# Kernel tuning notes

Measured on AMD Instinct MI355X. Metric: run time of the kernel, lower is better.

The kernel has to match this reference:

```python
import jax, jax.numpy as jnp
import numpy as np

GROUPS = 32
EPS = 1e-5


def setup_inputs() -> dict:
    key = jax.random.key(0)
    ks = jax.random.split(key, 4)
    b, c, h, w = 4, 256, 64, 64
    x = jax.random.normal(ks[0], (b, c, h, w), dtype=jnp.float32)
    gn_gamma = jnp.ones((c,), dtype=jnp.float32)
    gn_beta = jnp.zeros((c,), dtype=jnp.float32)
    # 1x1 convs are pointwise linear maps: store kernels as [out, in]
    w_qkv = jax.random.normal(ks[1], (3 * c, c), dtype=jnp.float32) * (1.0 / np.sqrt(c))
    b_qkv = jnp.zeros((3 * c,), dtype=jnp.float32)
    w_out = jax.random.normal(ks[2], (c, c), dtype=jnp.float32) * (1.0 / np.sqrt(c))
    b_out = jnp.zeros((c,), dtype=jnp.float32)
    return {"x": x, "gn_gamma": gn_gamma, "gn_beta": gn_beta,
            "w_qkv": w_qkv, "b_qkv": b_qkv, "w_out": w_out, "b_out": b_out}


def reference(x, gn_gamma, gn_beta, w_qkv, b_qkv, w_out, b_out):
    b, c, h, w = x.shape
    # GroupNorm(32, c)
    xg = x.reshape(b, GROUPS, c // GROUPS, h, w)
    mean = jnp.mean(xg, axis=(2, 3, 4), keepdims=True)
    var = jnp.var(xg, axis=(2, 3, 4), keepdims=True)
    xn = ((xg - mean) * jax.lax.rsqrt(var + EPS)).reshape(b, c, h, w)
    xn = xn * gn_gamma[None, :, None, None] + gn_beta[None, :, None, None]
    # 1x1 conv QKV projection: [b, 3c, h, w]
    qkv = jnp.einsum('bchw,oc->bohw', xn, w_qkv) + b_qkv[None, :, None, None]
    q, k, v = jnp.split(qkv, 3, axis=1)
    n = h * w
    q = q.transpose(0, 2, 3, 1).reshape(b, n, c)  # [b, n, c]
    k = k.reshape(b, c, n)                        # [b, c, n]
    v = v.transpose(0, 2, 3, 1).reshape(b, n, c)  # [b, n, c]
    scores = jnp.einsum('bic,bcj->bij', q, k) * (c ** -0.5)  # [b, n, n]
    attn = jax.nn.softmax(scores, axis=-1)
    out = jnp.einsum('bij,bjc->bic', attn, v)     # [b, n, c]
    out = out.reshape(b, h, w, c).transpose(0, 3, 1, 2)  # [b, c, h, w]
    out = jnp.einsum('bchw,oc->bohw', out, w_out) + b_out[None, :, None, None]
    return out + x
```

## Files before the change

### kernel.cpp

```cpp
#include <hip/hip_runtime.h>
#include <hip/hip_bf16.h>
#include <cstdint>
#include <cstddef>

#define DEVINL __device__ __forceinline__

typedef unsigned short u16;
typedef unsigned char u8;
typedef unsigned int u32;
typedef __attribute__((ext_vector_type(8))) short short8;
typedef __attribute__((ext_vector_type(4))) float f32x4;
typedef __attribute__((ext_vector_type(4))) u16 u16x4;

constexpr int CH = 256;
constexpr int HW = 4096;
constexpr int NB = 4;
constexpr float M0L = 5.7707801636f;
constexpr float QKS = 0.3002805f;

DEVINL u16 f2bf(float f) {
  union { float f; u32 u; } v; v.f = f;
  u32 u = v.u;
  u32 r = u + 0x7FFFu + ((u >> 16) & 1u);
  return (u16)(r >> 16);
}
DEVINL float bf2f(u16 h) {
  union { u32 u; float f; } v; v.u = ((u32)h) << 16; return v.f;
}
DEVINL float fexp2(float x) {
  float r; asm("v_exp_f32 %0, %1" : "=v"(r) : "v"(x)); return r;
}
DEVINL u32 cvtpk(float lo, float hi) {
  u32 r; asm("v_cvt_pk_bf16_f32 %0, %1, %2" : "=v"(r) : "v"(lo), "v"(hi)); return r;
}
DEVINL u8 f2fp8(float v) {
  return (u8)(__builtin_amdgcn_cvt_pk_fp8_f32(v, v, 0, false) & 0xFF);
}
DEVINL void plswap(u32& a, u32& b) {
  asm("v_permlane32_swap_b32 %0, %1" : "+v"(a), "+v"(b));
  asm("v_permlane16_swap_b32 %0, %1" : "+v"(a), "+v"(b));
}

DEVINL void gl_lds16(const void* g, void* l) {
  __builtin_amdgcn_global_load_lds(
      (__attribute__((address_space(1))) void*)(size_t)g,
      (__attribute__((address_space(3))) void*)l, 16, 0, 0);
}

DEVINL f32x4 mfma_bf16(short8 a, short8 b, f32x4 c) {
  return __builtin_amdgcn_mfma_f32_16x16x32_bf16(a, b, c, 0, 0, 0);
}
DEVINL f32x4 mfma_fp8(long a, long b, f32x4 c) {
  return __builtin_amdgcn_mfma_f32_16x16x32_fp8_fp8(a, b, c, 0, 0, 0);
}

__global__ void k_pre(const float* __restrict__ x, float* __restrict__ stats,
                      const float* __restrict__ wq, const float* __restrict__ wo,
                      u16* __restrict__ w3, u16* __restrict__ wob) {
  if (blockIdx.x >= 128) {
    int i = (blockIdx.x - 128) * 256 + threadIdx.x;
    w3[i] = f2bf(wq[i]);
    if (i < 65536) wob[i] = f2bf(wo[i]);
    return;
  }
  int bg = blockIdx.x;
  const float* p = x + (size_t)bg * 32768;
  float s = 0.f, ss = 0.f;
  for (int i = threadIdx.x; i < 8192; i += 256) {
    float4 v = ((const float4*)p)[i];
    s += v.x + v.y + v.z + v.w;
    ss += v.x * v.x + v.y * v.y + v.z * v.z + v.w * v.w;
  }
  for (int m = 32; m; m >>= 1) { s += __shfl_xor(s, m); ss += __shfl_xor(ss, m); }
  __shared__ float rs[4], rss[4];
  int w = threadIdx.x >> 6;
  if ((threadIdx.x & 63) == 0) { rs[w] = s; rss[w] = ss; }
  __syncthreads();
  if (threadIdx.x == 0) {
    s = rs[0] + rs[1] + rs[2] + rs[3];
    ss = rss[0] + rss[1] + rss[2] + rss[3];
    float mean = s / 32768.f;
    float var = ss / 32768.f - mean * mean;
    stats[bg * 2] = mean;
    stats[bg * 2 + 1] = rsqrtf(var + 1e-5f);
  }
}

__global__ void k_norm(const float* __restrict__ x, const float* __restrict__ stats,
                       const float* __restrict__ gamma, const float* __restrict__ beta,
                       u16* __restrict__ xnT) {
  int bid = blockIdx.x;
  int b = bid >> 8, ct = (bid >> 6) & 3, pt = bid & 63;
  int c0 = ct * 64, p0 = pt * 64;
  __shared__ u16 tile[64][66];
  const float* xb = x + ((size_t)b * CH + c0) * HW + p0;
#pragma unroll
  for (int it = 0; it < 4; it++) {
    int li = threadIdx.x + it * 256;
    int ci = li >> 4, pq = (li & 15) * 4;
    float4 v = *(const float4*)(xb + (size_t)ci * HW + pq);
    int c = c0 + ci;
    int gg = c >> 3;
    float mean = stats[(b * 32 + gg) * 2], rstd = stats[(b * 32 + gg) * 2 + 1];
    float ga = gamma[c] * rstd;
    float be = beta[c] - mean * ga;
    tile[ci][pq + 0] = f2bf(v.x * ga + be);
    tile[ci][pq + 1] = f2bf(v.y * ga + be);
    tile[ci][pq + 2] = f2bf(v.z * ga + be);
    tile[ci][pq + 3] = f2bf(v.w * ga + be);
  }
  __syncthreads();
#pragma unroll
  for (int it = 0; it < 2; it++) {
    int ch = threadIdx.x + it * 256;
    int pr = ch >> 3, cc = (ch & 7) * 8;
    short8 res;
#pragma unroll
    for (int q2 = 0; q2 < 8; q2++) res[q2] = (short)tile[cc + q2][pr];
    *(short8*)(xnT + ((size_t)b * HW + p0 + pr) * CH + c0 + cc) = res;
  }
}

DEVINL void stage_tile(char* dst, const u16* src_rows, int kt, int w, int lane) {
#pragma unroll
  for (int it = 0; it < 4; it++) {
    int CI = w * 256 + it * 64 + lane;
    int row = CI >> 3, ci = CI & 7;
    int sci = ci ^ (row & 7);
    gl_lds16(src_rows + (size_t)row * 256 + kt * 64 + sci * 8,
             dst + w * 4096 + it * 1024);
  }
}

DEVINL short8 ldsA(const char* base, int row, int colb) {
  return *(const short8*)(base + row * 128 + (colb ^ ((row & 7) << 4)));
}

__global__ __launch_bounds__(256, 2) void k_qkv(
    const u16* __restrict__ xnT, const u16* __restrict__ w3,
    const float* __restrict__ bqkv,
    u8* __restrict__ Qg8, u8* __restrict__ Kg8, u16* __restrict__ Vg) {
  int bid = blockIdx.x;
  int b = bid / 192; int rm = bid - b * 192; int mt = rm / 6, nt = rm - mt * 6;
  extern __shared__ char sm[];
  const int tid = threadIdx.x, w = tid >> 6, lane = tid & 63, t = lane & 15, g = lane >> 4;
  const u16* Abase = xnT + ((size_t)b * HW + mt * 128) * CH;
  const u16* Bbase = w3 + (size_t)nt * 128 * CH;
  f32x4 acc[4][4] = {};
  stage_tile(sm, Abase, 0, w, lane);
  stage_tile(sm + 32768, Bbase, 0, w, lane);
  __syncthreads();
  for (int kt = 0; kt < 4; kt++) {
    int cur = kt & 1;
    if (kt < 3) {
      stage_tile(sm + ((cur ^ 1) * 16384), Abase, kt + 1, w, lane);
      stage_tile(sm + 32768 + ((cur ^ 1) * 16384), Bbase, kt + 1, w, lane);
    }
    const char* Asm = sm + cur * 16384;
    const char* Bsm = sm + 32768 + cur * 16384;
#pragma unroll
    for (int ks = 0; ks < 2; ks++) {
      short8 af[4], bf[4];
#pragma unroll
      for (int m = 0; m < 4; m++) af[m] = ldsA(Asm, 64 * (w >> 1) + 16 * m + t, ks * 64 + g * 16);
#pragma unroll
      for (int n = 0; n < 4; n++) bf[n] = ldsA(Bsm, 64 * (w & 1) + 16 * n + t, ks * 64 + g * 16);
#pragma unroll
      for (int m = 0; m < 4; m++)
#pragma unroll
        for (int n = 0; n < 4; n++)
          acc[m][n] = mfma_bf16(af[m], bf[n], acc[m][n]);
    }
    __syncthreads();
  }
#pragma unroll
  for (int n = 0; n < 4; n++) {
    int o = nt * 128 + 64 * (w & 1) + 16 * n + t;
    float bias = bqkv[o];
#pragma unroll
    for (int m = 0; m < 4; m++) {
      int p0 = mt * 128 + 64 * (w >> 1) + 16 * m + 4 * g;
      if (nt < 4) {
        u8* dst = (nt < 2) ? Qg8 : Kg8;
        int oo = (nt < 2) ? o : o - 256;
#pragma unroll
        for (int rr = 0; rr < 4; rr++) {
          float v = (acc[m][n][rr] + bias) * QKS;
          dst[((size_t)b * HW + p0 + rr) * CH + oo] = f2fp8(v);
        }
      } else {
        int oo = o - 512;
        u16x4 pv;
#pragma unroll
        for (int rr = 0; rr < 4; rr++) pv[rr] = f2bf(acc[m][n][rr] + bias);
        *(u16x4*)(Vg + (size_t)b * CH * HW + (size_t)oo * HW + p0) = pv;
      }
    }
  }
}

__global__ __launch_bounds__(512, 2) void k_attn(
    const u8* __restrict__ Qg8, const u8* __restrict__ Kg8, const u16* __restrict__ Vg,
    u16* __restrict__ Op, float* __restrict__ ml) {
  int bid = blockIdx.x;
  int qb = bid >> 4, b = (bid >> 2) & 3, split = bid & 3;
  extern __shared__ char sm[];
  const int tid = threadIdx.x, w = tid >> 6, lane = tid & 63, t = lane & 15, g = lane >> 4;
  const u8* Qb = Qg8 + (size_t)b * HW * CH;
  const u8* Kb = Kg8 + (size_t)b * HW * CH;
  const u16* Vb = Vg + (size_t)b * CH * HW;
  int qrow0 = qb * 256 + w * 32;
  int kv0 = split * 1024;

  long q8[2][8];
#pragma unroll
  for (int rf = 0; rf < 2; rf++)
#pragma unroll
    for (int ks = 0; ks < 8; ks++)
      q8[rf][ks] = *(const long*)(Qb + (size_t)(qrow0 + rf * 16 + t) * CH + ks * 32 + g * 8);

  f32x4 oacc[2][16] = {};
  float lsum[2] = {0.f, 0.f};
  f32x4 sf[2][4];
  short8 pf[2][2];

  int kOffB[2], vOffE[4];
#pragma unroll
  for (int it = 0; it < 2; it++) {
    int CI = w * 128 + it * 64 + lane;
    int row = CI >> 4, c = CI & 15;
    kOffB[it] = row * 256 + ((c ^ (row & 7)) * 16);
  }
#pragma unroll
  for (int it = 0; it < 4; it++) {
    int CI = w * 256 + it * 64 + lane;
    int rowv = CI >> 3, civ = CI & 7;
    vOffE[it] = rowv * HW + ((civ ^ (rowv & 7)) * 8);
  }
  auto stageKV = [&](int kbuf, int vbuf, int tt) {
    char* KL = sm + kbuf * 16384 + w * 2048;
    char* VL = sm + 32768 + vbuf * 32768 + w * 4096;
    const u8* ksrc = Kb + (size_t)(kv0 + tt * 64) * CH;
    const u16* vsrc = Vb + (kv0 + tt * 64);
#pragma unroll
    for (int it = 0; it < 2; it++) gl_lds16(ksrc + kOffB[it], KL + it * 1024);
#pragma unroll
    for (int it = 0; it < 4; it++) gl_lds16(vsrc + vOffE[it], VL + it * 1024);
  };

  auto QK = [&](const char* KL) {
#pragma unroll
    for (int jf = 0; jf < 4; jf++) {
      int row = jf * 16 + t;
      f32x4 a0 = {}, a1 = {};
#pragma unroll
      for (int ks = 0; ks < 8; ks++) {
        int s = ks * 4 + g;
        long kf = *(const long*)(KL + row * 256 + (((s >> 1) ^ (row & 7)) << 4) + ((s & 1) << 3));
        a0 = mfma_fp8(kf, q8[0][ks], a0);
        a1 = mfma_fp8(kf, q8[1][ks], a1);
      }
      sf[0][jf] = a0; sf[1][jf] = a1;
    }
  };
  auto PV = [&](const char* VL) {
#pragma unroll
    for (int ks = 0; ks < 2; ks++)
#pragma unroll
      for (int cf = 0; cf < 16; cf++) {
        int row = cf * 16 + t;
        short8 vf = *(const short8*)(VL + row * 128 + ((ks * 64 + g * 16) ^ ((row & 7) << 4)));
        oacc[0][cf] = mfma_bf16(pf[0][ks], vf, oacc[0][cf]);
        oacc[1][cf] = mfma_bf16(pf[1][ks], vf, oacc[1][cf]);
      }
  };
  auto SM = [&]() {
#pragma unroll
    for (int rf = 0; rf < 2; rf++) {
      u32 A[4][2];
#pragma unroll
      for (int jf = 0; jf < 4; jf++) {
        float e0 = fexp2(sf[rf][jf][0] - M0L);
        float e1 = fexp2(sf[rf][jf][1] - M0L);
        float e2 = fexp2(sf[rf][jf][2] - M0L);
        float e3 = fexp2(sf[rf][jf][3] - M0L);
        lsum[rf] += (e0 + e1) + (e2 + e3);
        A[jf][0] = cvtpk(e0, e1);
        A[jf][1] = cvtpk(e2, e3);
      }
#pragma unroll
      for (int ks = 0; ks < 2; ks++) {
        u32 X0 = A[2 * ks][0], Y0 = A[2 * ks + 1][0];
        u32 X1 = A[2 * ks][1], Y1 = A[2 * ks + 1][1];
        plswap(X0, Y0);
        plswap(X1, Y1);
        union { u32 u[4]; short8 s8; } pk;
        pk.u[0] = X0; pk.u[1] = X1; pk.u[2] = Y0; pk.u[3] = Y1;
        pf[rf][ks] = pk.s8;
      }
    }
  };

  stageKV(0, 0, 0);
  stageKV(1, 1, 1);
  asm volatile("s_waitcnt vmcnt(6)" ::: "memory");
  __builtin_amdgcn_s_barrier();
  __builtin_amdgcn_sched_barrier(0);
  __builtin_amdgcn_s_setprio(1);
  QK(sm + 0);
  __builtin_amdgcn_s_setprio(0);
  __builtin_amdgcn_s_barrier();
  SM();

  for (int tt = 1; tt < 16; tt++) {
    int kcur = tt & 1, vprv = (tt - 1) % 3, vnxt = (tt + 1) % 3;
    stageKV(kcur ^ 1, vnxt, (tt + 1) & 15);
    asm volatile("s_waitcnt vmcnt(6)" ::: "memory");
    __builtin_amdgcn_s_barrier();
    __builtin_amdgcn_sched_barrier(0);
    __builtin_amdgcn_s_setprio(1);
    PV(sm + 32768 + vprv * 32768);
    QK(sm + kcur * 16384);
    __builtin_amdgcn_s_setprio(0);
    __builtin_amdgcn_s_barrier();
    __builtin_amdgcn_sched_barrier(0);
    SM();
  }
  __builtin_amdgcn_s_setprio(1);
  PV(sm + 32768 + (15 % 3) * 32768);
  __builtin_amdgcn_s_setprio(0);

  size_t obase = (size_t)(split * NB + b) * HW;
#pragma unroll
  for (int rf = 0; rf < 2; rf++) {
#pragma unroll
    for (int cf = 0; cf < 16; cf++)
#pragma unroll
      for (int rr = 0; rr < 4; rr++) {
        int row = qrow0 + rf * 16 + 4 * g + rr;
        Op[(obase + row) * CH + cf * 16 + t] = f2bf(oacc[rf][cf][rr]);
      }
    float ls = lsum[rf];
    ls += __shfl_xor(ls, 16);
    ls += __shfl_xor(ls, 32);
    if (g == 0) ml[obase + qrow0 + rf * 16 + t] = ls;
  }
}

__global__ __launch_bounds__(256, 2) void k_oproj(
    const u16* __restrict__ wob, const u16* __restrict__ Op, const float* __restrict__ ml,
    const float* __restrict__ bout, const float* __restrict__ x,
    float* __restrict__ out) {
  int bid = blockIdx.x;
  int b = bid >> 6, mt = (bid >> 5) & 1, nt = bid & 31;
  extern __shared__ char sm[];
  const int tid = threadIdx.x, w = tid >> 6, lane = tid & 63, t = lane & 15, g = lane >> 4;
  const u16* Abase = wob + (size_t)mt * 128 * CH;

  auto stageB = [&](char* dst, int kt) {
#pragma unroll
    for (int it = 0; it < 4; it++) {
      int CI = w * 256 + it * 64 + lane;
      int row = CI >> 3, ci = CI & 7;
      int sci = ci ^ (row & 7);
      int p = nt * 128 + row;
      float l = 0.f;
      float accv[8] = {};
#pragma unroll
      for (int s = 0; s < 4; s++) {
        size_t r = (size_t)(s * NB + b) * HW + p;
        l += ml[r];
        short8 a = *(const short8*)(Op + r * CH + kt * 64 + sci * 8);
#pragma unroll
        for (int q2 = 0; q2 < 8; q2++) accv[q2] += bf2f((u16)a[q2]);
      }
      float inv = 1.f / l;
      short8 res;
#pragma unroll
      for (int q2 = 0; q2 < 8; q2++) res[q2] = (short)f2bf(accv[q2] * inv);
      *(short8*)(dst + CI * 16) = res;
    }
  };

  f32x4 acc[4][4] = {};
  stage_tile(sm, Abase, 0, w, lane);
  stageB(sm + 32768, 0);
  __syncthreads();
  for (int kt = 0; kt < 4; kt++) {
    int cur = kt & 1;
    if (kt < 3) {
      stage_tile(sm + ((cur ^ 1) * 16384), Abase, kt + 1, w, lane);
      stageB(sm + 32768 + ((cur ^ 1) * 16384), kt + 1);
    }
    const char* Asm = sm + cur * 16384;
    const char* Bsm = sm + 32768 + cur * 16384;
#pragma unroll
    for (int ks = 0; ks < 2; ks++) {
      short8 af[4], bf[4];
#pragma unroll
      for (int m = 0; m < 4; m++) af[m] = ldsA(Asm, 64 * (w >> 1) + 16 * m + t, ks * 64 + g * 16);
#pragma unroll
      for (int n = 0; n < 4; n++) bf[n] = ldsA(Bsm, 64 * (w & 1) + 16 * n + t, ks * 64 + g * 16);
#pragma unroll
      for (int m = 0; m < 4; m++)
#pragma unroll
        for (int n = 0; n < 4; n++)
          acc[m][n] = mfma_bf16(af[m], bf[n], acc[m][n]);
    }
    __syncthreads();
  }
#pragma unroll
  for (int m = 0; m < 4; m++) {
    int o0 = mt * 128 + 64 * (w >> 1) + 16 * m + 4 * g;
#pragma unroll
    for (int n = 0; n < 4; n++) {
      int p = nt * 128 + 64 * (w & 1) + 16 * n + t;
#pragma unroll
      for (int rr = 0; rr < 4; rr++) {
        int o = o0 + rr;
        size_t off = ((size_t)b * CH + o) * HW + p;
        out[off] = acc[m][n][rr] + bout[o] + x[off];
      }
    }
  }
}

extern "C" void kernel_launch(void* const* d_in, const int* in_sizes, int n_in,
                              void* d_out, int out_size, void* d_ws, size_t ws_size,
                              hipStream_t stream) {
  const float* x = (const float*)d_in[0];
  const float* gamma = (const float*)d_in[1];
  const float* beta = (const float*)d_in[2];
  const float* wqkv = (const float*)d_in[3];
  const float* bqkv = (const float*)d_in[4];
  const float* wout = (const float*)d_in[5];
  const float* bout = (const float*)d_in[6];
  float* out = (float*)d_out;
  char* ws = (char*)d_ws;

  float* stats = (float*)(ws);
  u16* w3 = (u16*)(ws + 1024);
  u16* wob = (u16*)(ws + 1024 + 393216);
  u16* xnT = (u16*)(ws + 525312);
  u8* Qg8 = (u8*)(ws + 525312 + 1ull * 8388608);
  u8* Kg8 = (u8*)(ws + 525312 + 1ull * 8388608 + 4194304);
  u16* Vg = (u16*)(ws + 525312 + 2ull * 8388608);
  u16* Op = (u16*)(ws + 525312 + 3ull * 8388608);
  float* ml = (float*)(ws + 525312 + 7ull * 8388608);

  hipFuncSetAttribute(reinterpret_cast<const void*>(k_qkv),
                      hipFuncAttributeMaxDynamicSharedMemorySize, 65536);
  hipFuncSetAttribute(reinterpret_cast<const void*>(k_oproj),
                      hipFuncAttributeMaxDynamicSharedMemorySize, 65536);
  hipFuncSetAttribute(reinterpret_cast<const void*>(k_attn),
                      hipFuncAttributeMaxDynamicSharedMemorySize, 131072);

  k_pre<<<896, 256, 0, stream>>>(x, stats, wqkv, wout, w3, wob);
  k_norm<<<1024, 256, 0, stream>>>(x, stats, gamma, beta, xnT);
  k_qkv<<<768, 256, 65536, stream>>>(xnT, w3, bqkv, Qg8, Kg8, Vg);
  k_attn<<<256, 512, 131072, stream>>>(Qg8, Kg8, Vg, Op, ml);
  k_oproj<<<256, 256, 65536, stream>>>(wob, Op, ml, bout, x, out);
}
```

Baseline: 116.1 us.

## Store V and softmax probabilities in FP8 for the PV matmul

V is now written by the QKV projection as FP8 instead of bf16, and the attention kernel computes P·V with FP8 MFMA, packing the exponentiated scores directly into FP8. This halves V global and LDS traffic, shrinks LDS use from 128 KiB to 80 KiB per block, and uses the faster FP8 MFMA path. The LDS swizzle and fragment layout change to match. The cost is lower precision for both the probabilities and V, which could hurt accuracy tolerance.

```diff
diff --git a/kernel.cpp b/kernel.cpp
--- a/kernel.cpp
+++ b/kernel.cpp
@@ -8,6 +8,7 @@
 typedef unsigned short u16;
 typedef unsigned char u8;
 typedef unsigned int u32;
+typedef unsigned long long u64;
 typedef __attribute__((ext_vector_type(8))) short short8;
 typedef __attribute__((ext_vector_type(4))) float f32x4;
 typedef __attribute__((ext_vector_type(4))) u16 u16x4;
@@ -30,11 +31,13 @@
 DEVINL float fexp2(float x) {
   float r; asm("v_exp_f32 %0, %1" : "=v"(r) : "v"(x)); return r;
 }
-DEVINL u32 cvtpk(float lo, float hi) {
-  u32 r; asm("v_cvt_pk_bf16_f32 %0, %1, %2" : "=v"(r) : "v"(lo), "v"(hi)); return r;
-}
 DEVINL u8 f2fp8(float v) {
   return (u8)(__builtin_amdgcn_cvt_pk_fp8_f32(v, v, 0, false) & 0xFF);
+}
+DEVINL u32 pk4fp8(float v0, float v1, float v2, float v3) {
+  int r = __builtin_amdgcn_cvt_pk_fp8_f32(v0, v1, 0, false);
+  r = __builtin_amdgcn_cvt_pk_fp8_f32(v2, v3, r, true);
+  return (u32)r;
 }
 DEVINL void plswap(u32& a, u32& b) {
   asm("v_permlane32_swap_b32 %0, %1" : "+v"(a), "+v"(b));
@@ -139,7 +142,7 @@
 __global__ __launch_bounds__(256, 2) void k_qkv(
     const u16* __restrict__ xnT, const u16* __restrict__ w3,
     const float* __restrict__ bqkv,
-    u8* __restrict__ Qg8, u8* __restrict__ Kg8, u16* __restrict__ Vg) {
+    u8* __restrict__ Qg8, u8* __restrict__ Kg8, u8* __restrict__ Vg8) {
   int bid = blockIdx.x;
   int b = bid / 192; int rm = bid - b * 192; int mt = rm / 6, nt = rm - mt * 6;
   extern __shared__ char sm[];
@@ -190,17 +193,16 @@
         }
       } else {
         int oo = o - 512;
-        u16x4 pv;
-#pragma unroll
-        for (int rr = 0; rr < 4; rr++) pv[rr] = f2bf(acc[m][n][rr] + bias);
-        *(u16x4*)(Vg + (size_t)b * CH * HW + (size_t)oo * HW + p0) = pv;
+        u32 pv = pk4fp8(acc[m][n][0] + bias, acc[m][n][1] + bias,
+                        acc[m][n][2] + bias, acc[m][n][3] + bias);
+        *(u32*)(Vg8 + (size_t)b * CH * HW + (size_t)oo * HW + p0) = pv;
       }
     }
   }
 }
 
 __global__ __launch_bounds__(512, 2) void k_attn(
-    const u8* __restrict__ Qg8, const u8* __restrict__ Kg8, const u16* __restrict__ Vg,
+    const u8* __restrict__ Qg8, const u8* __restrict__ Kg8, const u8* __restrict__ Vg8,
     u16* __restrict__ Op, float* __restrict__ ml) {
   int bid = blockIdx.x;
   int qb = bid >> 4, b = (bid >> 2) & 3, split = bid & 3;
@@ -208,7 +210,7 @@
   const int tid = threadIdx.x, w = tid >> 6, lane = tid & 63, t = lane & 15, g = lane >> 4;
   const u8* Qb = Qg8 + (size_t)b * HW * CH;
   const u8* Kb = Kg8 + (size_t)b * HW * CH;
-  const u16* Vb = Vg + (size_t)b * CH * HW;
+  const u8* Vb = Vg8 + (size_t)b * CH * HW;
   int qrow0 = qb * 256 + w * 32;
   int kv0 = split * 1024;
 
@@ -222,30 +224,26 @@
   f32x4 oacc[2][16] = {};
   float lsum[2] = {0.f, 0.f};
   f32x4 sf[2][4];
-  short8 pf[2][2];
-
-  int kOffB[2], vOffE[4];
+  long pf[2][2];
+
+  int kOffB[2], vOffB[2];
 #pragma unroll
   for (int it = 0; it < 2; it++) {
     int CI = w * 128 + it * 64 + lane;
     int row = CI >> 4, c = CI & 15;
     kOffB[it] = row * 256 + ((c ^ (row & 7)) * 16);
-  }
-#pragma unroll
-  for (int it = 0; it < 4; it++) {
-    int CI = w * 256 + it * 64 + lane;
-    int rowv = CI >> 3, civ = CI & 7;
-    vOffE[it] = rowv * HW + ((civ ^ (rowv & 7)) * 8);
+    int rv = CI >> 2, c4 = CI & 3;
+    vOffB[it] = rv * HW + ((c4 ^ ((rv >> 1) & 3)) * 16);
   }
   auto stageKV = [&](int kbuf, int vbuf, int tt) {
     char* KL = sm + kbuf * 16384 + w * 2048;
-    char* VL = sm + 32768 + vbuf * 32768 + w * 4096;
+    char* VL = sm + 32768 + vbuf * 16384 + w * 2048;
     const u8* ksrc = Kb + (size_t)(kv0 + tt * 64) * CH;
-    const u16* vsrc = Vb + (kv0 + tt * 64);
+    const u8* vsrc = Vb + (kv0 + tt * 64);
 #pragma unroll
     for (int it = 0; it < 2; it++) gl_lds16(ksrc + kOffB[it], KL + it * 1024);
 #pragma unroll
-    for (int it = 0; it < 4; it++) gl_lds16(vsrc + vOffE[it], VL + it * 1024);
+    for (int it = 0; it < 2; it++) gl_lds16(vsrc + vOffB[it], VL + it * 1024);
   };
 
   auto QK = [&](const char* KL) {
@@ -269,15 +267,16 @@
 #pragma unroll
       for (int cf = 0; cf < 16; cf++) {
         int row = cf * 16 + t;
-        short8 vf = *(const short8*)(VL + row * 128 + ((ks * 64 + g * 16) ^ ((row & 7) << 4)));
-        oacc[0][cf] = mfma_bf16(pf[0][ks], vf, oacc[0][cf]);
-        oacc[1][cf] = mfma_bf16(pf[1][ks], vf, oacc[1][cf]);
+        long vf = *(const long*)(VL + row * 64 +
+                    (((ks * 2 + (g >> 1)) ^ ((row >> 1) & 3)) << 4) + ((g & 1) << 3));
+        oacc[0][cf] = mfma_fp8(pf[0][ks], vf, oacc[0][cf]);
+        oacc[1][cf] = mfma_fp8(pf[1][ks], vf, oacc[1][cf]);
       }
   };
   auto SM = [&]() {
 #pragma unroll
     for (int rf = 0; rf < 2; rf++) {
-      u32 A[4][2];
+      u32 A4[4];
 #pragma unroll
       for (int jf = 0; jf < 4; jf++) {
         float e0 = fexp2(sf[rf][jf][0] - M0L);
@@ -285,25 +284,20 @@
         float e2 = fexp2(sf[rf][jf][2] - M0L);
         float e3 = fexp2(sf[rf][jf][3] - M0L);
         lsum[rf] += (e0 + e1) + (e2 + e3);
-        A[jf][0] = cvtpk(e0, e1);
-        A[jf][1] = cvtpk(e2, e3);
+        A4[jf] = pk4fp8(e0, e1, e2, e3);
       }
 #pragma unroll
       for (int ks = 0; ks < 2; ks++) {
-        u32 X0 = A[2 * ks][0], Y0 = A[2 * ks + 1][0];
-        u32 X1 = A[2 * ks][1], Y1 = A[2 * ks + 1][1];
-        plswap(X0, Y0);
-        plswap(X1, Y1);
-        union { u32 u[4]; short8 s8; } pk;
-        pk.u[0] = X0; pk.u[1] = X1; pk.u[2] = Y0; pk.u[3] = Y1;
-        pf[rf][ks] = pk.s8;
+        u32 X = A4[2 * ks], Y = A4[2 * ks + 1];
+        plswap(X, Y);
+        pf[rf][ks] = (long)(((u64)Y << 32) | X);
       }
     }
   };
 
   stageKV(0, 0, 0);
   stageKV(1, 1, 1);
-  asm volatile("s_waitcnt vmcnt(6)" ::: "memory");
+  asm volatile("s_waitcnt vmcnt(4)" ::: "memory");
   __builtin_amdgcn_s_barrier();
   __builtin_amdgcn_sched_barrier(0);
   __builtin_amdgcn_s_setprio(1);
@@ -315,11 +309,11 @@
   for (int tt = 1; tt < 16; tt++) {
     int kcur = tt & 1, vprv = (tt - 1) % 3, vnxt = (tt + 1) % 3;
     stageKV(kcur ^ 1, vnxt, (tt + 1) & 15);
-    asm volatile("s_waitcnt vmcnt(6)" ::: "memory");
+    asm volatile("s_waitcnt vmcnt(4)" ::: "memory");
     __builtin_amdgcn_s_barrier();
     __builtin_amdgcn_sched_barrier(0);
     __builtin_amdgcn_s_setprio(1);
-    PV(sm + 32768 + vprv * 32768);
+    PV(sm + 32768 + vprv * 16384);
     QK(sm + kcur * 16384);
     __builtin_amdgcn_s_setprio(0);
     __builtin_amdgcn_s_barrier();
@@ -327,7 +321,7 @@
     SM();
   }
   __builtin_amdgcn_s_setprio(1);
-  PV(sm + 32768 + (15 % 3) * 32768);
+  PV(sm + 32768 + (15 % 3) * 16384);
   __builtin_amdgcn_s_setprio(0);
 
   size_t obase = (size_t)(split * NB + b) * HW;
@@ -444,7 +438,7 @@
   u16* xnT = (u16*)(ws + 525312);
   u8* Qg8 = (u8*)(ws + 525312 + 1ull * 8388608);
   u8* Kg8 = (u8*)(ws + 525312 + 1ull * 8388608 + 4194304);
-  u16* Vg = (u16*)(ws + 525312 + 2ull * 8388608);
+  u8* Vg8 = (u8*)(ws + 525312 + 2ull * 8388608);
   u16* Op = (u16*)(ws + 525312 + 3ull * 8388608);
   float* ml = (float*)(ws + 525312 + 7ull * 8388608);
 
@@ -453,11 +447,11 @@
   hipFuncSetAttribute(reinterpret_cast<const void*>(k_oproj),
                       hipFuncAttributeMaxDynamicSharedMemorySize, 65536);
   hipFuncSetAttribute(reinterpret_cast<const void*>(k_attn),
-                      hipFuncAttributeMaxDynamicSharedMemorySize, 131072);
+                      hipFuncAttributeMaxDynamicSharedMemorySize, 81920);
 
   k_pre<<<896, 256, 0, stream>>>(x, stats, wqkv, wout, w3, wob);
   k_norm<<<1024, 256, 0, stream>>>(x, stats, gamma, beta, xnT);
-  k_qkv<<<768, 256, 65536, stream>>>(xnT, w3, bqkv, Qg8, Kg8, Vg);
-  k_attn<<<256, 512, 131072, stream>>>(Qg8, Kg8, Vg, Op, ml);
+  k_qkv<<<768, 256, 65536, stream>>>(xnT, w3, bqkv, Qg8, Kg8, Vg8);
+  k_attn<<<256, 512, 81920, stream>>>(Qg8, Kg8, Vg8, Op, ml);
   k_oproj<<<256, 256, 65536, stream>>>(wob, Op, ml, bout, x, out);
 }
```

Result: no change. 115.3 us (-0.7%).
